# Kernel tuning notes

Measured on AMD Instinct MI355X. Metric: run time of the kernel, lower is better.

## Reference

```python
import jax, jax.numpy as jnp
import numpy as np

EPS = 1e-5
TEMP = 0.2  # contrastive temperature


def setup_inputs() -> dict:
    key = jax.random.key(0)
    ks_ = jax.random.split(key, 16)
    N, d, d_free, D, F_ = 10000, 32, 32, 64, 3
    x = jax.random.normal(ks_[0], (N, 256), dtype=jnp.float32)
    feats = jax.random.normal(ks_[1], (F_, N, d), dtype=jnp.float32)
    feat_free = 0.01 * jax.random.normal(ks_[2], (N, d_free), dtype=jnp.float32)
    # curvatures: k = init_curvature * randn(); keep away from 0 so the curved branch is taken
    ks = jax.random.uniform(ks_[3], (F_,), dtype=jnp.float32) + 0.5
    Ws = jax.random.normal(ks_[4], (F_, D, d), dtype=jnp.float32)
    Ws = Ws / jnp.linalg.norm(Ws, axis=-1, keepdims=True)  # row-normalized as in __init__
    bias = 2.0 * jnp.pi * jax.random.uniform(ks_[5], (F_, D), dtype=jnp.float32)
    W_free = jax.random.normal(ks_[6], (D, d_free), dtype=jnp.float32)
    W_free = W_free / jnp.linalg.norm(W_free, axis=-1, keepdims=True)
    b_free = 2.0 * jnp.pi * jax.random.uniform(ks_[7], (D,), dtype=jnp.float32)
    W1 = 0.05 * jax.random.normal(ks_[8], (3 * d, 64), dtype=jnp.float32)
    b1 = jnp.zeros((64,), dtype=jnp.float32)
    W2 = 0.05 * jax.random.normal(ks_[9], (64, 1), dtype=jnp.float32)
    b2 = jnp.zeros((1,), dtype=jnp.float32)
    motif = jax.random.randint(ks_[10], (3, 50000), 0, N, dtype=jnp.int32)
    neg_uv = jax.random.randint(ks_[11], (2, 50000), 0, N, dtype=jnp.int32)
    return {"x": x, "feats": feats, "feat_free": feat_free, "ks": ks,
            "Ws": Ws, "bias": bias, "W_free": W_free, "b_free": b_free,
            "W1": W1, "b1": b1, "W2": W2, "b2": b2,
            "motif": motif, "neg_uv": neg_uv}


def _normalize(xf, k):
    # RiemannianFeatures.normalize with the random scale fixed at 0.5 for determinism
    radius = 1.0 / jnp.sqrt(jnp.abs(k))
    xn = jnp.linalg.norm(xf, axis=-1, keepdims=True)
    return xf / xn * (0.9 * 0.5) * radius


def _mlp(f3, W1, b1, W2, b2):
    return jax.nn.relu(f3 @ W1 + b1) @ W2 + b2  # [M, 1]


def _gather3(feat, m):
    # nodes_from_motif: concat features of u, v, w
    return jnp.concatenate([feat[m[0]], feat[m[1]], feat[m[2]]], axis=-1)


def reference(x, feats, feat_free, ks, Ws, bias, W_free, b_free,
              W1, b1, W2, b2, motif, neg_uv):
    F_, N, d = feats.shape
    d_free = feat_free.shape[-1]

    # ---- RiemannianFeatures.forward: normalized products per factor + free part
    products = [_normalize(feats[i], ks[i]) for i in range(F_)]
    products.append(feat_free)

    # ---- random_mapping: pairwise manifold distance -> exp/cos transform
    zs = []
    for i in range(F_):
        xi, w, b, k = products[i], Ws[i], bias[i], ks[i]
        div = jnp.sum((xi[:, None, :] - w[None, :, :]) ** 2, axis=-1)      # [N, D]
        num = 1.0 + k * jnp.sum(xi * xi, axis=-1, keepdims=True)           # [N, 1]
        dist = jnp.log(num / (div + EPS))
        zs.append(jnp.exp((d - 1) * dist * 0.5) * jnp.cos(dist + b))
    dist_f = feat_free @ W_free.T                                          # Euclidean branch
    zs.append(jnp.exp((d_free - 1) * dist_f * 0.5) * jnp.cos(dist_f + b_free))
    x2 = jnp.concatenate(zs, axis=-1)                                      # [N, embed]

    # ---- cal_cl_loss: full N x N cosine-similarity contrastive loss
    n1 = jnp.linalg.norm(x, axis=-1)
    n2 = jnp.linalg.norm(x2, axis=-1)
    sim = jnp.einsum('ik,jk->ij', x, x2) / (n1[:, None] * n2[None, :])
    sim = jnp.exp(sim / TEMP)
    pos = jnp.diagonal(sim)
    loss_1 = -jnp.mean(jnp.log(pos / (jnp.sum(sim, axis=0) - pos)))
    loss_2 = -jnp.mean(jnp.log(pos / (jnp.sum(sim, axis=1) - pos)))
    cl_loss = 0.5 * (loss_1 + loss_2)

    # ---- cal_motif_loss: gather triples -> MLP -> BCE (neg via provided sampled pairs)
    neg_motif = jnp.concatenate([neg_uv, motif[2:3]], axis=0)
    motif_loss = jnp.float32(0.0)
    for p in products:
        pos_logit = _mlp(_gather3(p, motif), W1, b1, W2, b2)
        neg_logit = _mlp(_gather3(p, neg_motif), W1, b1, W2, b2)
        motif_loss = motif_loss \
            - jnp.mean(jax.nn.log_sigmoid(pos_logit)) \
            - jnp.mean(jax.nn.log_sigmoid(-neg_logit))

    return cl_loss + motif_loss
```

## Files before the change

kernel.cpp:

```cpp
#include <hip/hip_runtime.h>
#include <hip/hip_bf16.h>
#include <math.h>

#define EMBED 256
#define NF 3
#define DD 64
#define BM 128
#define BN 128
#define BK 64
#define NKT 4
#define MOTIF_BLOCKS 2048
#define NE 512
#define NMLP 1024

typedef unsigned short ushort_t;
typedef unsigned char uchar_t;
typedef float f32x4 __attribute__((ext_vector_type(4)));
typedef float f32x2 __attribute__((ext_vector_type(2)));

__device__ __forceinline__ void gl2lds16(const void* g, void* l) {
    __builtin_amdgcn_global_load_lds(
        (const __attribute__((address_space(1))) unsigned int*)g,
        (__attribute__((address_space(3))) unsigned int*)l, 16, 0, 0);
}

__device__ __forceinline__ uchar_t f2fp8(float f) {
    int p = __builtin_amdgcn_cvt_pk_fp8_f32(f, f, 0, false);
    return (uchar_t)(p & 0xff);
}
template<bool HI>
__device__ __forceinline__ f32x2 pk2(unsigned int w) {
    return __builtin_amdgcn_cvt_pk_f32_fp8((int)w, HI);
}

__device__ __forceinline__ float dpp16_red_add(float x) {
    int v;
    v = __builtin_amdgcn_update_dpp(0, __float_as_int(x), 0xB1, 0xF, 0xF, true);
    x += __int_as_float(v);
    v = __builtin_amdgcn_update_dpp(0, __float_as_int(x), 0x4E, 0xF, 0xF, true);
    x += __int_as_float(v);
    v = __builtin_amdgcn_update_dpp(0, __float_as_int(x), 0x141, 0xF, 0xF, true);
    x += __int_as_float(v);
    v = __builtin_amdgcn_update_dpp(0, __float_as_int(x), 0x140, 0xF, 0xF, true);
    x += __int_as_float(v);
    return x;
}

__global__ __launch_bounds__(256) void k_pre(
    const float* __restrict__ x,
    const float* __restrict__ feats,
    const float* __restrict__ feat_free,
    const float* __restrict__ ks,
    const float* __restrict__ Ws,
    const float* __restrict__ bias,
    const float* __restrict__ W_free,
    const float* __restrict__ b_free,
    const float* __restrict__ W1,
    const float* __restrict__ b1,
    uchar_t* __restrict__ xnf8,
    uchar_t* __restrict__ x2nf8,
    uchar_t* __restrict__ H8,
    float* __restrict__ acc3,
    int N, int Npad)
{
    int tid = threadIdx.x;

    if (blockIdx.x >= NE) {
        int lane = tid & 63;
        int gw = ((blockIdx.x - NE) * 256 + tid) >> 6;
        int nwaves = (NMLP * 256) >> 6;

        float wcol[96];
        #pragma unroll
        for (int c = 0; c < 96; ++c) wcol[c] = W1[c*64 + lane];
        float b1l = b1[lane];
        float kv0 = ks[0], kv1 = ks[1], kv2 = ks[2];

        int total = 4 * N;
        for (int unit = gw; unit < total; unit += nwaves) {
            int node = __builtin_amdgcn_readfirstlane(unit >> 2);
            int prod = __builtin_amdgcn_readfirstlane(unit & 3);
            float fc[32];
            if (prod < 3) {
                const float* P = feats + ((size_t)prod*N + node)*32;
                float red[32];
                #pragma unroll
                for (int c = 0; c < 32; ++c) { fc[c] = P[c]; red[c] = fc[c]*fc[c]; }
                #pragma unroll
                for (int st = 1; st < 32; st <<= 1)
                    #pragma unroll
                    for (int c = 0; c < 32; c += 2*st) red[c] = red[c] + red[c + st];
                float s = red[0];
                float k = (prod == 0) ? kv0 : (prod == 1) ? kv1 : kv2;
                float scale = 0.45f / (sqrtf(s) * sqrtf(fabsf(k)));
                #pragma unroll
                for (int c = 0; c < 32; ++c) fc[c] *= scale;
            } else {
                const float* P = feat_free + (size_t)node*32;
                #pragma unroll
                for (int c = 0; c < 32; ++c) fc[c] = P[c];
            }
            #pragma unroll
            for (int s = 0; s < 3; ++s) {
                float h = (s == 2) ? b1l : 0.f;
                #pragma unroll
                for (int c = 0; c < 32; ++c) h = fmaf(fc[c], wcol[s*32 + c], h);
                H8[(((size_t)prod*3 + s)*N + node)*64 + lane] = f2fp8(h);
            }
        }
        return;
    }

    int wave = tid >> 6;
    int t    = tid & 63;
    int gtid = blockIdx.x * 256 + tid;
    int stride = NE * 256;

    for (int i = gtid; i < 4; i += stride) acc3[i] = 0.f;
    {
        int pad = (Npad - N) * (EMBED/4);
        int* pa = (int*)(xnf8  + (size_t)N*EMBED);
        int* pb = (int*)(x2nf8 + (size_t)N*EMBED);
        for (int i = gtid; i < pad; i += stride) { pa[i] = 0; pb[i] = 0; }
    }

    __shared__ float Wl[128*65];
    __shared__ float xi_s[4][NF][32];
    __shared__ float ff_s[4][32];

    for (int e = tid; e < NF*DD*32; e += 256) {
        int i = e >> 11, rem = e & 2047, tr = rem >> 5, c = rem & 31;
        Wl[(i*32 + c)*65 + tr] = Ws[e];
    }
    for (int e = tid; e < DD*32; e += 256) {
        int tr = e >> 5, c = e & 31;
        Wl[(96 + c)*65 + tr] = W_free[e];
    }
    __syncthreads();

    float (*xi)[32] = xi_s[wave];
    float* ffs = ff_s[wave];
    int ngroups = (N + 3) >> 2;

    for (int grp = blockIdx.x; grp < ngroups; grp += NE) {
        int n = grp*4 + wave;
        if (n >= N) continue;

        float v[NF];
        float ffv = 0.f;
        if (t < 32) {
            #pragma unroll
            for (int i = 0; i < NF; ++i) v[i] = feats[((size_t)i*N + n)*32 + t];
            ffv = feat_free[(size_t)n*32 + t];
        } else {
            #pragma unroll
            for (int i = 0; i < NF; ++i) v[i] = 0.f;
        }

        float num[NF];
        #pragma unroll
        for (int i = 0; i < NF; ++i) {
            float s = v[i]*v[i];
            s += __shfl_xor(s, 1, 64);  s += __shfl_xor(s, 2, 64);
            s += __shfl_xor(s, 4, 64);  s += __shfl_xor(s, 8, 64);
            s += __shfl_xor(s, 16, 64);
            s = __shfl(s, 0, 64);
            float k = ks[i];
            float scale = 0.45f / (sqrtf(s) * sqrtf(fabsf(k)));
            float xv = v[i] * scale;
            if (t < 32) xi[i][t] = xv;
            num[i] = 1.0f + k * (scale*scale*s);
        }
        if (t < 32) ffs[t] = ffv;

        float z[4];
        float zsq = 0.f;
        #pragma unroll
        for (int i = 0; i < NF; ++i) {
            float div = 0.f;
            #pragma unroll
            for (int c = 0; c < 32; ++c) {
                float d = xi[i][c] - Wl[(i*32 + c)*65 + t];
                div += d*d;
            }
            float dist = __logf(num[i] / (div + 1e-5f));
            float zz = __expf(15.5f * dist) * __cosf(dist + bias[i*DD + t]);
            z[i] = zz;
            zsq += zz*zz;
        }
        {
            float dot = 0.f;
            #pragma unroll
            for (int c = 0; c < 32; ++c) dot = fmaf(ffs[c], Wl[(96 + c)*65 + t], dot);
            float zz = __expf(15.5f * dot) * __cosf(dot + b_free[t]);
            z[3] = zz;
            zsq += zz*zz;
        }
        zsq += __shfl_xor(zsq, 1, 64);  zsq += __shfl_xor(zsq, 2, 64);
        zsq += __shfl_xor(zsq, 4, 64);  zsq += __shfl_xor(zsq, 8, 64);
        zsq += __shfl_xor(zsq, 16, 64); zsq += __shfl_xor(zsq, 32, 64);
        float iv2 = 1.0f / sqrtf(zsq);

        #pragma unroll
        for (int i = 0; i < NF; ++i) x2nf8[(size_t)n*EMBED + i*DD + t] = f2fp8(z[i]*iv2);
        x2nf8[(size_t)n*EMBED + 192 + t] = f2fp8(z[3]*iv2);

        float xv[4];
        float s1 = 0.f;
        #pragma unroll
        for (int q = 0; q < 4; ++q) { xv[q] = x[(size_t)n*EMBED + q*64 + t]; s1 += xv[q]*xv[q]; }
        s1 += __shfl_xor(s1, 1, 64);  s1 += __shfl_xor(s1, 2, 64);
        s1 += __shfl_xor(s1, 4, 64);  s1 += __shfl_xor(s1, 8, 64);
        s1 += __shfl_xor(s1, 16, 64); s1 += __shfl_xor(s1, 32, 64);
        float iv1 = 5.0f / sqrtf(s1);
        #pragma unroll
        for (int q = 0; q < 4; ++q) xnf8[(size_t)n*EMBED + q*64 + t] = f2fp8(xv[q]*iv1);
    }
}

__global__ __launch_bounds__(256, 4) void k_fused(
    const uchar_t* __restrict__ xn, const uchar_t* __restrict__ x2n,
    const uchar_t* __restrict__ H,
    const int* __restrict__ motif,
    const int* __restrict__ neg_uv,
    const float* __restrict__ W2,
    const float* __restrict__ b2,
    float* __restrict__ rowpart,
    float* __restrict__ colpart,
    float* __restrict__ pos,
    float* __restrict__ partials,
    int N, int Npad, int nb, int M)
{
    __shared__ __align__(16) uchar_t smem[2*(BM*BK + BN*BK)];

    if (blockIdx.x < MOTIF_BLOCKS) {
        float* wred = (float*)smem;
        int lane = threadIdx.x & 63;
        int sub  = lane >> 3;
        int ch   = (lane & 7) * 8;
        int caseId = blockIdx.x & 7;
        int rank   = (blockIdx.x >> 3) * 4 + (threadIdx.x >> 6);
        int prod  = caseId >> 1;
        int isneg = caseId & 1;
        const uchar_t* Hu = H + ((size_t)prod*3 + 0)*N*64;
        const uchar_t* Hv = H + ((size_t)prod*3 + 1)*N*64;
        const uchar_t* Hw = H + ((size_t)prod*3 + 2)*N*64;
        const int* iu = isneg ? neg_uv       : motif;
        const int* iv = isneg ? (neg_uv + M) : (motif + M);
        const int* iw = motif + 2*M;

        float w2c[8];
        #pragma unroll
        for (int c = 0; c < 8; ++c) w2c[c] = W2[ch + c];
        float b2v = b2[0];

        float accl = 0.f;
        #pragma unroll 2
        for (int r0 = rank*8; r0 < M; r0 += 8192) {
            int r = r0 + sub;
            bool ok = (r < M);
            int rc = ok ? r : 0;
            int u = iu[rc], v = iv[rc], w = iw[rc];
            uint2 du = *(const uint2*)&Hu[(size_t)u*64 + ch];
            uint2 dv = *(const uint2*)&Hv[(size_t)v*64 + ch];
            uint2 dw = *(const uint2*)&Hw[(size_t)w*64 + ch];
            float pl = 0.f;
            {
                f32x2 s;
                s = pk2<false>(du.x) + pk2<false>(dv.x) + pk2<false>(dw.x);
                pl = fmaf(fmaxf(s.x,0.f), w2c[0], pl);  pl = fmaf(fmaxf(s.y,0.f), w2c[1], pl);
                s = pk2<true>(du.x) + pk2<true>(dv.x) + pk2<true>(dw.x);
                pl = fmaf(fmaxf(s.x,0.f), w2c[2], pl);  pl = fmaf(fmaxf(s.y,0.f), w2c[3], pl);
                s = pk2<false>(du.y) + pk2<false>(dv.y) + pk2<false>(dw.y);
                pl = fmaf(fmaxf(s.x,0.f), w2c[4], pl);  pl = fmaf(fmaxf(s.y,0.f), w2c[5], pl);
                s = pk2<true>(du.y) + pk2<true>(dv.y) + pk2<true>(dw.y);
                pl = fmaf(fmaxf(s.x,0.f), w2c[6], pl);  pl = fmaf(fmaxf(s.y,0.f), w2c[7], pl);
            }
            pl += __shfl_xor(pl, 1, 64);
            pl += __shfl_xor(pl, 2, 64);
            pl += __shfl_xor(pl, 4, 64);
            float logit = pl + b2v;
            float z = isneg ? -logit : logit;
            float sp = fmaxf(-z, 0.f) + __logf(1.f + __expf(-fabsf(z)));
            accl -= ok ? sp : 0.f;
        }
        #pragma unroll
        for (int m = 1; m < 64; m <<= 1) accl += __shfl_xor(accl, m, 64);

        if (lane == 0) wred[threadIdx.x >> 6] = accl;
        __syncthreads();
        if (threadIdx.x == 0)
            partials[blockIdx.x] = (wred[0] + wred[1] + wred[2] + wred[3]) * 0.125f;
        return;
    }

    int tid  = threadIdx.x;
    int lane = tid & 63;
    int w    = tid >> 6;
    int wr   = w >> 1, wc = w & 1;
    int quad = lane >> 4, l15 = lane & 15;

    int pid = blockIdx.x - MOTIF_BLOCKS;
    int nwg = nb * nb;
    int qq = nwg >> 3, rr = nwg & 7;
    int xcd = pid & 7, idx = pid >> 3;
    int wg = (xcd < rr ? xcd*(qq+1) : rr*(qq+1) + (xcd-rr)*qq) + idx;

    int per_group = 8 * nb;
    int group = wg / per_group;
    int rem = wg - group * per_group;
    int rowspan = min(8, nb - group * 8);
    int prow = group * 8 + rem % rowspan;
    int pcol = rem / rowspan;
    int row0 = prow * BM, col0 = pcol * BN;

    f32x4 acc[4][4];
    #pragma unroll
    for (int i = 0; i < 4; ++i)
        #pragma unroll
        for (int j = 0; j < 4; ++j) acc[i][j] = (f32x4){0.f,0.f,0.f,0.f};

    auto stage = [&](int t) {
        uchar_t* A = smem + (t & 1) * (BM*BK + BN*BK);
        uchar_t* B = A + BM*BK;
        int k0 = t * BK;
        #pragma unroll
        for (int i = 0; i < 2; ++i) {
            int slot = i*256 + tid;
            int r = slot >> 2, c = slot & 3;
            int sc = c ^ ((r >> 1) & 3);
            gl2lds16(xn  + (size_t)(row0 + r)*EMBED + k0 + sc*16, &A[slot*16]);
            gl2lds16(x2n + (size_t)(col0 + r)*EMBED + k0 + sc*16, &B[slot*16]);
        }
    };

    stage(0);
    stage(1);

    #pragma unroll
    for (int kt = 0; kt < NKT; ++kt) {
        if (kt == NKT-1) asm volatile("s_waitcnt vmcnt(0)" ::: "memory");
        else             asm volatile("s_waitcnt vmcnt(4)" ::: "memory");
        __builtin_amdgcn_s_barrier();

        const uchar_t* A = smem + (kt & 1) * (BM*BK + BN*BK);
        const uchar_t* B = A + BM*BK;
        #pragma unroll
        for (int s = 0; s < 2; ++s) {
            long a[4], b[4];
            int cq = s*2 + (quad >> 1);
            int h8 = (quad & 1) * 8;
            #pragma unroll
            for (int ti = 0; ti < 4; ++ti) {
                int ra = wr*64 + ti*16 + l15;
                a[ti] = *(const long*)&A[ra*BK + ((cq ^ ((ra >> 1) & 3)) << 4) + h8];
            }
            #pragma unroll
            for (int tj = 0; tj < 4; ++tj) {
                int rb = wc*64 + tj*16 + l15;
                b[tj] = *(const long*)&B[rb*BK + ((cq ^ ((rb >> 1) & 3)) << 4) + h8];
            }
            __builtin_amdgcn_s_setprio(1);
            #pragma unroll
            for (int ti = 0; ti < 4; ++ti)
                #pragma unroll
                for (int tj = 0; tj < 4; ++tj)
                    acc[ti][tj] = __builtin_amdgcn_mfma_f32_16x16x32_fp8_fp8(a[ti], b[tj], acc[ti][tj], 0, 0, 0);
            __builtin_amdgcn_s_setprio(0);
        }
        if (kt + 2 < NKT) {
            __builtin_amdgcn_s_barrier();
            stage(kt + 2);
        }
    }
    __syncthreads();

    float* rsum_s = (float*)smem;
    float* csum_s = rsum_s + 2*BM;

    bool edge = (prow == nb-1) || (pcol == nb-1);
    float csv[4] = {0.f, 0.f, 0.f, 0.f};

    if (!edge) {
        bool diagb = (prow == pcol) && (wr == wc);
        #pragma unroll
        for (int ti = 0; ti < 4; ++ti) {
            #pragma unroll
            for (int r = 0; r < 4; ++r) {
                float rs = 0.f;
                #pragma unroll
                for (int tj = 0; tj < 4; ++tj) {
                    float e = __expf(acc[ti][tj][r]);
                    rs += e;
                    csv[tj] += e;
                    if (tj == ti && diagb && l15 == quad*4 + r)
                        pos[row0 + wr*64 + ti*16 + quad*4 + r] = e;
                }
                rs = dpp16_red_add(rs);
                if (l15 == 0) rsum_s[wc*BM + wr*64 + ti*16 + quad*4 + r] = rs;
            }
        }
    } else {
        #pragma unroll
        for (int ti = 0; ti < 4; ++ti) {
            #pragma unroll
            for (int r = 0; r < 4; ++r) {
                int gi = row0 + wr*64 + ti*16 + quad*4 + r;
                float rs = 0.f;
                #pragma unroll
                for (int tj = 0; tj < 4; ++tj) {
                    int gj = col0 + wc*64 + tj*16 + l15;
                    float e = 0.f;
                    if (gi < N && gj < N) {
                        e = __expf(acc[ti][tj][r]);
                        if (gi == gj) pos[gi] = e;
                    }
                    rs += e;
                    csv[tj] += e;
                }
                rs = dpp16_red_add(rs);
                if (l15 == 0) rsum_s[wc*BM + wr*64 + ti*16 + quad*4 + r] = rs;
            }
        }
    }
    #pragma unroll
    for (int tj = 0; tj < 4; ++tj) {
        float cs = csv[tj];
        cs += __shfl_xor(cs, 16, 64);
        cs += __shfl_xor(cs, 32, 64);
        if (lane < 16) csum_s[wr*BM + wc*64 + tj*16 + lane] = cs;
    }
    __syncthreads();
    if (tid < BM) {
        rowpart[(size_t)pcol*Npad + row0 + tid] = rsum_s[tid] + rsum_s[BM + tid];
        colpart[(size_t)prow*Npad + col0 + tid] = csum_s[tid] + csum_s[BM + tid];
    }
}

__global__ __launch_bounds__(256) void k_final(
    const float* __restrict__ rowpart, const float* __restrict__ colpart,
    const float* __restrict__ pos, const float* __restrict__ partials,
    float* __restrict__ acc3, int* __restrict__ ticket,
    float* __restrict__ out, int N, int Npad, int nb, int nparts, int M)
{
    __shared__ float red1[256], red2[256], red3[256];
    int t = threadIdx.x;
    int g = blockIdx.x * 256 + t;
    int stride = gridDim.x * 256;
    float l1 = 0.f, l2 = 0.f, mo = 0.f;
    for (int i = g; i < N; i += stride) {
        float rs = 0.f, cs = 0.f;
        for (int p = 0; p < nb; ++p) {
            rs += rowpart[(size_t)p*Npad + i];
            cs += colpart[(size_t)p*Npad + i];
        }
        float pv = pos[i];
        l1 += __logf((cs - pv) / pv);
        l2 += __logf((rs - pv) / pv);
    }
    for (int i = g; i < nparts; i += stride) mo += partials[i];
    red1[t] = l1; red2[t] = l2; red3[t] = mo; __syncthreads();
    for (int s = 128; s > 0; s >>= 1) {
        if (t < s) { red1[t] += red1[t+s]; red2[t] += red2[t+s]; red3[t] += red3[t+s]; }
        __syncthreads();
    }
    if (t == 0) {
        atomicAdd(&acc3[0], red1[0]);
        atomicAdd(&acc3[1], red2[0]);
        atomicAdd(&acc3[2], red3[0]);
        __threadfence();
        int old = atomicAdd(ticket, 1);
        if (old == (int)gridDim.x - 1) {
            float a0 = atomicAdd(&acc3[0], 0.f);
            float a1 = atomicAdd(&acc3[1], 0.f);
            float a2 = atomicAdd(&acc3[2], 0.f);
            float cl = 0.5f * (a0 + a1) / (float)N;
            out[0] = cl - a2 / (float)M;
        }
    }
}

extern "C" void kernel_launch(void* const* d_in, const int* in_sizes, int n_in,
                              void* d_out, int out_size, void* d_ws, size_t ws_size,
                              hipStream_t stream)
{
    const float* x         = (const float*)d_in[0];
    const float* feats     = (const float*)d_in[1];
    const float* feat_free = (const float*)d_in[2];
    const float* ks        = (const float*)d_in[3];
    const float* Ws        = (const float*)d_in[4];
    const float* bias      = (const float*)d_in[5];
    const float* W_free    = (const float*)d_in[6];
    const float* b_free    = (const float*)d_in[7];
    const float* W1        = (const float*)d_in[8];
    const float* b1        = (const float*)d_in[9];
    const float* W2        = (const float*)d_in[10];
    const float* b2        = (const float*)d_in[11];
    const int*   motif     = (const int*)d_in[12];
    const int*   neg_uv    = (const int*)d_in[13];
    int N = in_sizes[0] / EMBED;
    int M = in_sizes[13] / 2;
    int nb = (N + BM - 1) / BM;
    int Npad = nb * BM;

    uchar_t* xnf8  = (uchar_t*)d_ws;
    uchar_t* x2nf8 = xnf8 + (size_t)Npad*EMBED;
    uchar_t* H8    = x2nf8 + (size_t)Npad*EMBED;
    float* posv   = (float*)(H8 + (size_t)12*N*64);
    float* acc3   = posv + N;
    int*   ticket = (int*)(acc3 + 3);
    float* partials = acc3 + 4;
    float* rowpart  = partials + MOTIF_BLOCKS;
    float* colpart  = rowpart + (size_t)nb*Npad;

    k_pre<<<NE + NMLP, 256, 0, stream>>>(x, feats, feat_free, ks, Ws, bias,
                                         W_free, b_free, W1, b1,
                                         xnf8, x2nf8, H8, acc3, N, Npad);
    k_fused<<<MOTIF_BLOCKS + nb*nb, 256, 0, stream>>>(xnf8, x2nf8, H8, motif, neg_uv,
                                                      W2, b2, rowpart, colpart, posv,
                                                      partials, N, Npad, nb, M);
    k_final<<<256, 256, 0, stream>>>(rowpart, colpart, posv, partials, acc3, ticket,
                                     (float*)d_out, N, Npad, nb, MOTIF_BLOCKS, M);
}
```

Before: 224.4 us.

## Load full-K tiles into LDS at once instead of double-buffered K pipeline

Replaces the double-buffered BK=64 staging loop with a single bulk load of the full 256-wide K extent for both A and B tiles into LDS, followed by one barrier and an unpipelined MFMA loop over 8 sub-steps. The XOR swizzle changes to a 16-way pattern to match the wider rows. This removes per-stage waitcnt/barrier overhead, but LDS use rises from 32KB to 64KB per block. That can lower occupancy, since launch_bounds asks for 4 blocks per CU, and it gives up overlap of loads with compute.

```diff
diff --git a/kernel.cpp b/kernel.cpp
--- a/kernel.cpp
+++ b/kernel.cpp
@@ -7,8 +7,6 @@
 #define DD 64
 #define BM 128
 #define BN 128
-#define BK 64
-#define NKT 4
 #define MOTIF_BLOCKS 2048
 #define NE 512
 #define NMLP 1024
@@ -231,7 +229,7 @@
     float* __restrict__ partials,
     int N, int Npad, int nb, int M)
 {
-    __shared__ __align__(16) uchar_t smem[2*(BM*BK + BN*BK)];
+    __shared__ __align__(16) uchar_t smem[BM*EMBED + BN*EMBED];
 
     if (blockIdx.x < MOTIF_BLOCKS) {
         float* wred = (float*)smem;
@@ -294,6 +292,9 @@
         return;
     }
 
+    uchar_t* As = smem;
+    uchar_t* Bs = smem + BM*EMBED;
+
     int tid  = threadIdx.x;
     int lane = tid & 63;
     int w    = tid >> 6;
@@ -314,64 +315,44 @@
     int pcol = rem / rowspan;
     int row0 = prow * BM, col0 = pcol * BN;
 
+    #pragma unroll
+    for (int i = 0; i < 8; ++i) {
+        int slot = i*256 + tid;
+        int r = slot >> 4, c = slot & 15;
+        int sc = c ^ (r & 15);
+        gl2lds16(xn  + (size_t)(row0 + r)*EMBED + sc*16, &As[slot*16]);
+        gl2lds16(x2n + (size_t)(col0 + r)*EMBED + sc*16, &Bs[slot*16]);
+    }
+    __syncthreads();
+
     f32x4 acc[4][4];
     #pragma unroll
     for (int i = 0; i < 4; ++i)
         #pragma unroll
         for (int j = 0; j < 4; ++j) acc[i][j] = (f32x4){0.f,0.f,0.f,0.f};
 
-    auto stage = [&](int t) {
-        uchar_t* A = smem + (t & 1) * (BM*BK + BN*BK);
-        uchar_t* B = A + BM*BK;
-        int k0 = t * BK;
-        #pragma unroll
-        for (int i = 0; i < 2; ++i) {
-            int slot = i*256 + tid;
-            int r = slot >> 2, c = slot & 3;
-            int sc = c ^ ((r >> 1) & 3);
-            gl2lds16(xn  + (size_t)(row0 + r)*EMBED + k0 + sc*16, &A[slot*16]);
-            gl2lds16(x2n + (size_t)(col0 + r)*EMBED + k0 + sc*16, &B[slot*16]);
-        }
-    };
-
-    stage(0);
-    stage(1);
-
     #pragma unroll
-    for (int kt = 0; kt < NKT; ++kt) {
-        if (kt == NKT-1) asm volatile("s_waitcnt vmcnt(0)" ::: "memory");
-        else             asm volatile("s_waitcnt vmcnt(4)" ::: "memory");
-        __builtin_amdgcn_s_barrier();
-
-        const uchar_t* A = smem + (kt & 1) * (BM*BK + BN*BK);
-        const uchar_t* B = A + BM*BK;
-        #pragma unroll
-        for (int s = 0; s < 2; ++s) {
-            long a[4], b[4];
-            int cq = s*2 + (quad >> 1);
-            int h8 = (quad & 1) * 8;
-            #pragma unroll
-            for (int ti = 0; ti < 4; ++ti) {
-                int ra = wr*64 + ti*16 + l15;
-                a[ti] = *(const long*)&A[ra*BK + ((cq ^ ((ra >> 1) & 3)) << 4) + h8];
-            }
-            #pragma unroll
-            for (int tj = 0; tj < 4; ++tj) {
-                int rb = wc*64 + tj*16 + l15;
-                b[tj] = *(const long*)&B[rb*BK + ((cq ^ ((rb >> 1) & 3)) << 4) + h8];
-            }
-            __builtin_amdgcn_s_setprio(1);
-            #pragma unroll
-            for (int ti = 0; ti < 4; ++ti)
-                #pragma unroll
-                for (int tj = 0; tj < 4; ++tj)
-                    acc[ti][tj] = __builtin_amdgcn_mfma_f32_16x16x32_fp8_fp8(a[ti], b[tj], acc[ti][tj], 0, 0, 0);
-            __builtin_amdgcn_s_setprio(0);
-        }
-        if (kt + 2 < NKT) {
-            __builtin_amdgcn_s_barrier();
-            stage(kt + 2);
-        }
+    for (int s = 0; s < 8; ++s) {
+        long a[4], b[4];
+        int cq = s*2 + (quad >> 1);
+        int h8 = (quad & 1) * 8;
+        #pragma unroll
+        for (int ti = 0; ti < 4; ++ti) {
+            int ra = wr*64 + ti*16 + l15;
+            a[ti] = *(const long*)&As[ra*EMBED + ((cq ^ (ra & 15)) << 4) + h8];
+        }
+        #pragma unroll
+        for (int tj = 0; tj < 4; ++tj) {
+            int rb = wc*64 + tj*16 + l15;
+            b[tj] = *(const long*)&Bs[rb*EMBED + ((cq ^ (rb & 15)) << 4) + h8];
+        }
+        __builtin_amdgcn_s_setprio(1);
+        #pragma unroll
+        for (int ti = 0; ti < 4; ++ti)
+            #pragma unroll
+            for (int tj = 0; tj < 4; ++tj)
+                acc[ti][tj] = __builtin_amdgcn_mfma_f32_16x16x32_fp8_fp8(a[ti], b[tj], acc[ti][tj], 0, 0, 0);
+        __builtin_amdgcn_s_setprio(0);
     }
     __syncthreads();
 
```

New measurement: 238.6 us. 6.3% more time.
